# Performance work log

Hardware: AMD Instinct MI355X
Metric: run time of the kernel (lower is better)

Reference implementation:

```python
import jax, jax.numpy as jnp
import numpy as np

B, H, N, D = 4, 16, 2048, 64

def setup_inputs() -> dict:
    key = jax.random.key(0)
    kq, kk, kv = jax.random.split(key, 3)
    q = jax.random.normal(kq, (B, H, N, D), dtype=jnp.float32)
    k = jax.random.normal(kk, (B, H, N, D), dtype=jnp.float32)
    v = jax.random.normal(kv, (B, H, N, D), dtype=jnp.float32)
    return {"q": q, "k": k, "v": v}

def reference(q, k, v):
    scale = q.shape[-1] ** -0.5
    # sim: [b, h, i, j]
    sim = jnp.einsum('bhid,bhjd->bhij', q, k) * scale
    attn = jax.nn.softmax(sim, axis=-1)  # dropout p=0.0 -> identity
    out = jnp.einsum('bhij,bhjd->bhid', attn, v)
    return out
```

## Files before the change

### kernel.cpp

```cpp
#include <hip/hip_runtime.h>
#include <stdint.h>


#define NSEQ 2048
#define DH   64
#define BHN  64
#define NIT  32

typedef short bf16x8 __attribute__((ext_vector_type(8)));
typedef float f32x4  __attribute__((ext_vector_type(4)));
typedef float f32x16 __attribute__((ext_vector_type(16)));

__device__ __forceinline__ uint16_t f2bf(float x) {
    uint32_t u = __builtin_bit_cast(uint32_t, x);
    return (uint16_t)((u + 0x7fffu + ((u >> 16) & 1u)) >> 16);
}
__device__ __forceinline__ uint32_t pk2(float a, float b) {
    return (uint32_t)f2bf(a) | ((uint32_t)f2bf(b) << 16);
}

__global__ __launch_bounds__(256) void prepass(const float* __restrict__ K,
                                               const float* __restrict__ V,
                                               uint16_t* __restrict__ F) {
    __shared__ float T1[64 * 68];
    const int b = blockIdx.x, bh = b >> 5, kt = b & 31, t = threadIdx.x;
    const size_t gbase = ((size_t)bh * NSEQ + (size_t)kt * 64) * DH;
    const int n = t >> 2, d0 = (t & 3) * 16;
    #pragma unroll
    for (int i = 0; i < 4; ++i)
        *(float4*)&T1[n * 68 + d0 + i * 4] = *(const float4*)(V + gbase + n * 64 + d0 + i * 4);
    __syncthreads();
    uint16_t* out = F + (size_t)(bh * 32 + kt) * 8192;
    #pragma unroll
    for (int p = 0; p < 4; ++p) {
        const int e = p * 256 + t, c = e >> 6, l = e & 63;
        const int ll = l & 31, hh = l >> 5;
        float f[8];
        if (c < 8) {
            const int row = (c >> 2) * 32 + ll;
            const int col = hh * 8 + (c & 3) * 16;
            const float* kp = K + gbase + (size_t)row * 64 + col;
            float4 a = *(const float4*)(kp);
            float4 g = *(const float4*)(kp + 4);
            f[0] = a.x; f[1] = a.y; f[2] = a.z; f[3] = a.w;
            f[4] = g.x; f[5] = g.y; f[6] = g.z; f[7] = g.w;
        } else {
            const int cc = c - 8, ktg = cc >> 1;
            const int d = (cc & 1) * 32 + ll;
            #pragma unroll
            for (int j = 0; j < 8; ++j) {
                const int i = hh * 8 + j;
                const int s = (i & 3) + 8 * ((i >> 2) & 1) + 4 * ((i >> 3) & 1);
                f[j] = T1[(ktg * 16 + s) * 68 + d];
            }
        }
        uint4 o = make_uint4(pk2(f[0], f[1]), pk2(f[2], f[3]),
                             pk2(f[4], f[5]), pk2(f[6], f[7]));
        *(uint4*)(out + (size_t)c * 512 + l * 8) = o;
    }
}

__device__ __forceinline__ void load_q(const float* qp, float qscale, bf16x8 (&dst)[4]) {
    #pragma unroll
    for (int k2 = 0; k2 < 4; ++k2) {
        float4 a = *(const float4*)(qp + k2 * 16);
        float4 c = *(const float4*)(qp + k2 * 16 + 4);
        union { uint32_t u[4]; bf16x8 v; } pk;
        pk.u[0] = pk2(a.x * qscale, a.y * qscale);
        pk.u[1] = pk2(a.z * qscale, a.w * qscale);
        pk.u[2] = pk2(c.x * qscale, c.y * qscale);
        pk.u[3] = pk2(c.z * qscale, c.w * qscale);
        dst[k2] = pk.v;
    }
}

__device__ __forceinline__ void tile_nt(const uint4 (&kc)[4], const uint4 (&vc)[4],
                                        const bf16x8 (&qfn)[4],
                                        f32x16& o0, f32x16& o1, float& lsn) {
    f32x16 s = {};
    #pragma unroll
    for (int k2 = 0; k2 < 4; ++k2)
        s = __builtin_amdgcn_mfma_f32_32x32x16_bf16(
            __builtin_bit_cast(bf16x8, kc[k2]), qfn[k2], s, 0, 0, 0);
    bf16x8 pf0, pf1;
    float ls = 0.0f;
    {
        union { uint32_t u[4]; bf16x8 v; } pp;
        #pragma unroll
        for (int t2 = 0; t2 < 4; ++t2) {
            float e0 = __builtin_amdgcn_exp2f(s[2 * t2]);
            float e1 = __builtin_amdgcn_exp2f(s[2 * t2 + 1]);
            ls += e0 + e1;
            pp.u[t2] = __builtin_amdgcn_perm(
                __builtin_bit_cast(uint32_t, e1),
                __builtin_bit_cast(uint32_t, e0), 0x07060302u);
        }
        pf0 = pp.v;
    }
    {
        union { uint32_t u[4]; bf16x8 v; } pp;
        #pragma unroll
        for (int t2 = 0; t2 < 4; ++t2) {
            float e0 = __builtin_amdgcn_exp2f(s[8 + 2 * t2]);
            float e1 = __builtin_amdgcn_exp2f(s[8 + 2 * t2 + 1]);
            ls += e0 + e1;
            pp.u[t2] = __builtin_amdgcn_perm(
                __builtin_bit_cast(uint32_t, e1),
                __builtin_bit_cast(uint32_t, e0), 0x07060302u);
        }
        pf1 = pp.v;
    }
    lsn += ls;
    o0 = __builtin_amdgcn_mfma_f32_32x32x16_bf16(
        pf0, __builtin_bit_cast(bf16x8, vc[0]), o0, 0, 0, 0);
    o0 = __builtin_amdgcn_mfma_f32_32x32x16_bf16(
        pf1, __builtin_bit_cast(bf16x8, vc[2]), o0, 0, 0, 0);
    o1 = __builtin_amdgcn_mfma_f32_32x32x16_bf16(
        pf0, __builtin_bit_cast(bf16x8, vc[1]), o1, 0, 0, 0);
    o1 = __builtin_amdgcn_mfma_f32_32x32x16_bf16(
        pf1, __builtin_bit_cast(bf16x8, vc[3]), o1, 0, 0, 0);
}

__device__ __forceinline__ void ep_store(float (*XOd)[64], float* XLd,
                                         const f32x16& a0, const f32x16& a1,
                                         float ls, int lane) {
    #pragma unroll
    for (int e = 0; e < 16; ++e) XOd[e][lane] = a0[e];
    #pragma unroll
    for (int e = 0; e < 16; ++e) XOd[16 + e][lane] = a1[e];
    XLd[lane] = ls;
}
__device__ __forceinline__ void ep_add(const float (*XOs)[64],
                                       f32x16& a0, f32x16& a1, int lane) {
    #pragma unroll
    for (int e = 0; e < 16; ++e) a0[e] += XOs[e][lane];
    #pragma unroll
    for (int e = 0; e < 16; ++e) a1[e] += XOs[16 + e][lane];
}
__device__ __forceinline__ void ep_write(float* Ob, int row0,
                                         const f32x16& a0, const f32x16& a1,
                                         float lt, int l31, int h) {
    const float rinv = 1.0f / lt;
    const int rib = __builtin_bit_cast(int, rinv);
    #pragma unroll
    for (int rg = 0; rg < 16; ++rg) {
        const int il = (rg & 3) + 8 * (rg >> 2) + 4 * h;
        const float inv = __builtin_bit_cast(float,
            __builtin_amdgcn_ds_bpermute(il * 4, rib));
        const int row = row0 + il;
        Ob[(size_t)row * DH + l31]      = a0[rg] * inv;
        Ob[(size_t)row * DH + 32 + l31] = a1[rg] * inv;
    }
}

__global__ __launch_bounds__(128, 3) void attn_main(const float* __restrict__ Qg,
                                                    const uint16_t* __restrict__ F,
                                                    float* __restrict__ Og) {
    __shared__ float XO[2][32][64];
    __shared__ float XL[2][64];
    const int tid = threadIdx.x;
    const int w = tid >> 6, lane = tid & 63;
    const int l31 = lane & 31, h = lane >> 5;
    const int idx = blockIdx.x;
    const int bh = (idx & 7) * 8 + ((idx >> 3) & 7);
    const int qt = idx >> 6;

    const float qscale = 0.125f * 1.44269504f;
    bf16x8 qf0[4], qf1[4];
    {
        const float* qb = Qg + ((size_t)bh * NSEQ + (size_t)(qt * 64 + l31)) * DH + h * 8;
        load_q(qb, qscale, qf0);
        load_q(qb + 32 * DH, qscale, qf1);
    }

    f32x16 oa00 = {}, oa01 = {}, oa10 = {}, oa11 = {};
    float ls0 = 0.0f, ls1 = 0.0f;

    const uint16_t* fb = F + (size_t)bh * 32 * 8192 + (size_t)w * 2048 + (size_t)lane * 8;

    #pragma unroll 1
    for (int kt = 0; kt < NIT; ++kt) {
        uint4 kc[4], vc[4];
        #pragma unroll
        for (int c = 0; c < 4; ++c) kc[c] = *(const uint4*)(fb + (size_t)c * 512);
        #pragma unroll
        for (int c = 0; c < 4; ++c) vc[c] = *(const uint4*)(fb + (size_t)(8 + c) * 512);
        fb += 8192;
        tile_nt(kc, vc, qf0, oa00, oa01, ls0);
        tile_nt(kc, vc, qf1, oa10, oa11, ls1);
    }

    if (w == 0) ep_store(XO[0], XL[0], oa10, oa11, ls1, lane);
    else        ep_store(XO[1], XL[1], oa00, oa01, ls0, lane);
    __syncthreads();
    float lt;
    if (w == 0) { ep_add(XO[1], oa00, oa01, lane); lt = ls0 + XL[1][lane]; }
    else        { ep_add(XO[0], oa10, oa11, lane); lt = ls1 + XL[0][lane]; }
    lt += __shfl_xor(lt, 32);

    float* Ob = Og + (size_t)bh * NSEQ * DH;
    if (w == 0) ep_write(Ob, qt * 64,      oa00, oa01, lt, l31, h);
    else        ep_write(Ob, qt * 64 + 32, oa10, oa11, lt, l31, h);
}

#define LDS_S 72
#define NWAVE 4
#define BN    64
__global__ __launch_bounds__(256) void attn_fwd_fb(const float* __restrict__ Qg,
                                                   const float* __restrict__ Kg,
                                                   const float* __restrict__ Vg,
                                                   float* __restrict__ Og) {
    __shared__ short KsF[BN * LDS_S];
    __shared__ short VtsF[DH * LDS_S];
    __shared__ short PsF[NWAVE * 16 * LDS_S];
    const int tid = threadIdx.x;
    const int wave = tid >> 6, lane = tid & 63, quad = lane >> 4, l16 = lane & 15;
    const int bh = blockIdx.x >> 5, qtf = blockIdx.x & 31;
    const size_t base = (size_t)bh * NSEQ * DH;
    const float* Qb = Qg + base; const float* Kbf = Kg + base;
    const float* Vb = Vg + base; float* Ob = Og + base;
    const float qscale = 0.125f * 1.44269504f;
    bf16x8 qfrag[2];
    {
        const int qrow = qtf * 64 + wave * 16 + l16;
        const float* qp = Qb + (size_t)qrow * DH + quad * 8;
        #pragma unroll
        for (int c = 0; c < 2; ++c) {
            float4 x = *(const float4*)(qp + 32 * c);
            float4 y = *(const float4*)(qp + 32 * c + 4);
            union { uint16_t u[8]; bf16x8 v; } pk;
            pk.u[0]=f2bf(x.x*qscale); pk.u[1]=f2bf(x.y*qscale);
            pk.u[2]=f2bf(x.z*qscale); pk.u[3]=f2bf(x.w*qscale);
            pk.u[4]=f2bf(y.x*qscale); pk.u[5]=f2bf(y.y*qscale);
            pk.u[6]=f2bf(y.z*qscale); pk.u[7]=f2bf(y.w*qscale);
            qfrag[c] = pk.v;
        }
    }
    f32x4 o[4] = {};
    float m_i[4], l_i[4];
    #pragma unroll
    for (int r = 0; r < 4; ++r) { m_i[r] = -1e30f; l_i[r] = 0.0f; }
    const int kr0 = tid >> 4, kd0 = (tid & 15) * 4;
    const int vp = (tid & 31) * 2, vd0 = (tid >> 5) * 8;
    #pragma unroll 1
    for (int kt = 0; kt < NSEQ / BN; ++kt) {
        __syncthreads();
        {
            const float* kbase = Kbf + (size_t)kt * BN * DH;
            #pragma unroll
            for (int jj = 0; jj < 4; ++jj) {
                const int row = kr0 + jj * 16;
                float4 x = *(const float4*)(kbase + (size_t)row * DH + kd0);
                union { uint16_t u[4]; uint64_t ll; } pk;
                pk.u[0]=f2bf(x.x); pk.u[1]=f2bf(x.y); pk.u[2]=f2bf(x.z); pk.u[3]=f2bf(x.w);
                *(uint64_t*)&KsF[row * LDS_S + kd0] = pk.ll;
            }
        }
        {
            const float* v0 = Vb + (size_t)(kt * BN + vp) * DH + vd0;
            const float* v1 = v0 + DH;
            float4 a0 = *(const float4*)(v0); float4 a1 = *(const float4*)(v0 + 4);
            float4 b0 = *(const float4*)(v1); float4 b1 = *(const float4*)(v1 + 4);
            float av[8] = {a0.x,a0.y,a0.z,a0.w,a1.x,a1.y,a1.z,a1.w};
            float bv[8] = {b0.x,b0.y,b0.z,b0.w,b1.x,b1.y,b1.z,b1.w};
            #pragma unroll
            for (int i = 0; i < 8; ++i)
                *(uint32_t*)&VtsF[(vd0 + i) * LDS_S + vp] = pk2(av[i], bv[i]);
        }
        __syncthreads();
        f32x4 s[4] = {};
        #pragma unroll
        for (int c = 0; c < 2; ++c)
            #pragma unroll
            for (int n = 0; n < 4; ++n) {
                bf16x8 kfr = *(const bf16x8*)&KsF[(n * 16 + l16) * LDS_S + quad * 8 + 32 * c];
                s[n] = __builtin_amdgcn_mfma_f32_16x16x32_bf16(qfrag[c], kfr, s[n], 0, 0, 0);
            }
        float rmax[4];
        #pragma unroll
        for (int r = 0; r < 4; ++r)
            rmax[r] = fmaxf(fmaxf(s[0][r], s[1][r]), fmaxf(s[2][r], s[3][r]));
        #pragma unroll
        for (int off = 1; off < 16; off <<= 1)
            #pragma unroll
            for (int r = 0; r < 4; ++r)
                rmax[r] = fmaxf(rmax[r], __shfl_xor(rmax[r], off, 64));
        float alpha[4], rsum[4];
        #pragma unroll
        for (int r = 0; r < 4; ++r) {
            float mn = fmaxf(m_i[r], rmax[r]);
            alpha[r] = __builtin_amdgcn_exp2f(m_i[r] - mn);
            m_i[r] = mn; rsum[r] = 0.0f;
        }
        #pragma unroll
        for (int n = 0; n < 4; ++n)
            #pragma unroll
            for (int r = 0; r < 4; ++r) {
                float p = __builtin_amdgcn_exp2f(s[n][r] - m_i[r]);
                rsum[r] += p;
                PsF[(wave * 16 + quad * 4 + r) * LDS_S + n * 16 + l16] = (short)f2bf(p);
            }
        #pragma unroll
        for (int off = 1; off < 16; off <<= 1)
            #pragma unroll
            for (int r = 0; r < 4; ++r)
                rsum[r] += __shfl_xor(rsum[r], off, 64);
        #pragma unroll
        for (int r = 0; r < 4; ++r) l_i[r] = l_i[r] * alpha[r] + rsum[r];
        #pragma unroll
        for (int n = 0; n < 4; ++n)
            #pragma unroll
            for (int r = 0; r < 4; ++r) o[n][r] *= alpha[r];
        #pragma unroll
        for (int c = 0; c < 2; ++c) {
            bf16x8 pfr = *(const bf16x8*)&PsF[(wave * 16 + l16) * LDS_S + quad * 8 + 32 * c];
            #pragma unroll
            for (int n = 0; n < 4; ++n) {
                bf16x8 vfr = *(const bf16x8*)&VtsF[(n * 16 + l16) * LDS_S + quad * 8 + 32 * c];
                o[n] = __builtin_amdgcn_mfma_f32_16x16x32_bf16(pfr, vfr, o[n], 0, 0, 0);
            }
        }
    }
    float inv[4];
    #pragma unroll
    for (int r = 0; r < 4; ++r) inv[r] = 1.0f / l_i[r];
    const int orow0 = qtf * 64 + wave * 16 + quad * 4;
    #pragma unroll
    for (int n = 0; n < 4; ++n)
        #pragma unroll
        for (int r = 0; r < 4; ++r)
            Ob[(size_t)(orow0 + r) * DH + n * 16 + l16] = o[n][r] * inv[r];
}

extern "C" void kernel_launch(void* const* d_in, const int* in_sizes, int n_in,
                              void* d_out, int out_size, void* d_ws, size_t ws_size,
                              hipStream_t stream) {
    (void)in_sizes; (void)n_in; (void)out_size;
    const float* q = (const float*)d_in[0];
    const float* k = (const float*)d_in[1];
    const float* v = (const float*)d_in[2];
    float* out = (float*)d_out;
    const size_t need = (size_t)BHN * 32 * 16384;
    if (ws_size >= need) {
        uint16_t* fbuf = (uint16_t*)d_ws;
        prepass<<<dim3(BHN * 32), dim3(256), 0, stream>>>(k, v, fbuf);
        attn_main<<<dim3(2048), dim3(128), 0, stream>>>(q, fbuf, out);
    } else {
        attn_fwd_fb<<<dim3(BHN * 32), dim3(256), 0, stream>>>(q, k, v, out);
    }
}
```

Measured before the change: 210.0 us.

## Split query rows across waves instead of key tiles, dropping LDS reduction

Each wave now owns 32 query rows and walks all keys in the tile, rather than both waves sharing the query rows and splitting the key tile. This removes the shared-memory partial-sum exchange and the barrier in the epilogue, and halves the Q fragments and accumulators held per wave. In exchange each wave loads twice as much K/V per iteration, doubling global/L2 traffic per block and raising register pressure for the loaded tiles. The row-sum is also accumulated as a tree to shorten the dependency chain.

New measurement: 208.3 us. No clear change (-0.8%).

```diff
diff --git a/kernel.cpp b/kernel.cpp
--- a/kernel.cpp
+++ b/kernel.cpp
@@ -74,43 +74,45 @@
     }
 }
 
-__device__ __forceinline__ void tile_nt(const uint4 (&kc)[4], const uint4 (&vc)[4],
-                                        const bf16x8 (&qfn)[4],
-                                        f32x16& o0, f32x16& o1, float& lsn) {
+__device__ __forceinline__ void tile_mtj(const uint4 (&kc)[4], const uint4 (&vc)[4],
+                                         const bf16x8 (&qfn)[4],
+                                         f32x16& o0, f32x16& o1, float& lsn) {
     f32x16 s = {};
     #pragma unroll
     for (int k2 = 0; k2 < 4; ++k2)
         s = __builtin_amdgcn_mfma_f32_32x32x16_bf16(
             __builtin_bit_cast(bf16x8, kc[k2]), qfn[k2], s, 0, 0, 0);
     bf16x8 pf0, pf1;
-    float ls = 0.0f;
+    float g0, g1;
     {
         union { uint32_t u[4]; bf16x8 v; } pp;
+        float e[8];
         #pragma unroll
         for (int t2 = 0; t2 < 4; ++t2) {
-            float e0 = __builtin_amdgcn_exp2f(s[2 * t2]);
-            float e1 = __builtin_amdgcn_exp2f(s[2 * t2 + 1]);
-            ls += e0 + e1;
+            e[2 * t2]     = __builtin_amdgcn_exp2f(s[2 * t2]);
+            e[2 * t2 + 1] = __builtin_amdgcn_exp2f(s[2 * t2 + 1]);
             pp.u[t2] = __builtin_amdgcn_perm(
-                __builtin_bit_cast(uint32_t, e1),
-                __builtin_bit_cast(uint32_t, e0), 0x07060302u);
-        }
+                __builtin_bit_cast(uint32_t, e[2 * t2 + 1]),
+                __builtin_bit_cast(uint32_t, e[2 * t2]), 0x07060302u);
+        }
+        g0 = ((e[0] + e[1]) + (e[2] + e[3])) + ((e[4] + e[5]) + (e[6] + e[7]));
         pf0 = pp.v;
     }
     {
         union { uint32_t u[4]; bf16x8 v; } pp;
+        float e[8];
         #pragma unroll
         for (int t2 = 0; t2 < 4; ++t2) {
-            float e0 = __builtin_amdgcn_exp2f(s[8 + 2 * t2]);
-            float e1 = __builtin_amdgcn_exp2f(s[8 + 2 * t2 + 1]);
-            ls += e0 + e1;
+            e[2 * t2]     = __builtin_amdgcn_exp2f(s[8 + 2 * t2]);
+            e[2 * t2 + 1] = __builtin_amdgcn_exp2f(s[8 + 2 * t2 + 1]);
             pp.u[t2] = __builtin_amdgcn_perm(
-                __builtin_bit_cast(uint32_t, e1),
-                __builtin_bit_cast(uint32_t, e0), 0x07060302u);
-        }
+                __builtin_bit_cast(uint32_t, e[2 * t2 + 1]),
+                __builtin_bit_cast(uint32_t, e[2 * t2]), 0x07060302u);
+        }
+        g1 = ((e[0] + e[1]) + (e[2] + e[3])) + ((e[4] + e[5]) + (e[6] + e[7]));
         pf1 = pp.v;
     }
-    lsn += ls;
+    lsn += g0 + g1;
     o0 = __builtin_amdgcn_mfma_f32_32x32x16_bf16(
         pf0, __builtin_bit_cast(bf16x8, vc[0]), o0, 0, 0, 0);
     o0 = __builtin_amdgcn_mfma_f32_32x32x16_bf16(
@@ -121,22 +123,6 @@
         pf1, __builtin_bit_cast(bf16x8, vc[3]), o1, 0, 0, 0);
 }
 
-__device__ __forceinline__ void ep_store(float (*XOd)[64], float* XLd,
-                                         const f32x16& a0, const f32x16& a1,
-                                         float ls, int lane) {
-    #pragma unroll
-    for (int e = 0; e < 16; ++e) XOd[e][lane] = a0[e];
-    #pragma unroll
-    for (int e = 0; e < 16; ++e) XOd[16 + e][lane] = a1[e];
-    XLd[lane] = ls;
-}
-__device__ __forceinline__ void ep_add(const float (*XOs)[64],
-                                       f32x16& a0, f32x16& a1, int lane) {
-    #pragma unroll
-    for (int e = 0; e < 16; ++e) a0[e] += XOs[e][lane];
-    #pragma unroll
-    for (int e = 0; e < 16; ++e) a1[e] += XOs[16 + e][lane];
-}
 __device__ __forceinline__ void ep_write(float* Ob, int row0,
                                          const f32x16& a0, const f32x16& a1,
                                          float lt, int l31, int h) {
@@ -156,8 +142,6 @@
 __global__ __launch_bounds__(128, 3) void attn_main(const float* __restrict__ Qg,
                                                     const uint16_t* __restrict__ F,
                                                     float* __restrict__ Og) {
-    __shared__ float XO[2][32][64];
-    __shared__ float XL[2][64];
     const int tid = threadIdx.x;
     const int w = tid >> 6, lane = tid & 63;
     const int l31 = lane & 31, h = lane >> 5;
@@ -166,41 +150,34 @@
     const int qt = idx >> 6;
 
     const float qscale = 0.125f * 1.44269504f;
-    bf16x8 qf0[4], qf1[4];
-    {
-        const float* qb = Qg + ((size_t)bh * NSEQ + (size_t)(qt * 64 + l31)) * DH + h * 8;
-        load_q(qb, qscale, qf0);
-        load_q(qb + 32 * DH, qscale, qf1);
-    }
-
-    f32x16 oa00 = {}, oa01 = {}, oa10 = {}, oa11 = {};
-    float ls0 = 0.0f, ls1 = 0.0f;
-
-    const uint16_t* fb = F + (size_t)bh * 32 * 8192 + (size_t)w * 2048 + (size_t)lane * 8;
+    bf16x8 qf[4];
+    load_q(Qg + ((size_t)bh * NSEQ + (size_t)(qt * 64 + w * 32 + l31)) * DH + h * 8,
+           qscale, qf);
+
+    f32x16 oa0 = {}, oa1 = {};
+    float ls = 0.0f;
+
+    const uint16_t* fb = F + (size_t)bh * 32 * 8192 + (size_t)lane * 8;
 
     #pragma unroll 1
     for (int kt = 0; kt < NIT; ++kt) {
-        uint4 kc[4], vc[4];
-        #pragma unroll
-        for (int c = 0; c < 4; ++c) kc[c] = *(const uint4*)(fb + (size_t)c * 512);
-        #pragma unroll
-        for (int c = 0; c < 4; ++c) vc[c] = *(const uint4*)(fb + (size_t)(8 + c) * 512);
+        uint4 kcl[4], kch[4], vcl[4], vch[4];
+        #pragma unroll
+        for (int c = 0; c < 4; ++c) kcl[c] = *(const uint4*)(fb + (size_t)c * 512);
+        #pragma unroll
+        for (int c = 0; c < 4; ++c) kch[c] = *(const uint4*)(fb + (size_t)(4 + c) * 512);
+        #pragma unroll
+        for (int c = 0; c < 4; ++c) vcl[c] = *(const uint4*)(fb + (size_t)(8 + c) * 512);
+        #pragma unroll
+        for (int c = 0; c < 4; ++c) vch[c] = *(const uint4*)(fb + (size_t)(12 + c) * 512);
         fb += 8192;
-        tile_nt(kc, vc, qf0, oa00, oa01, ls0);
-        tile_nt(kc, vc, qf1, oa10, oa11, ls1);
-    }
-
-    if (w == 0) ep_store(XO[0], XL[0], oa10, oa11, ls1, lane);
-    else        ep_store(XO[1], XL[1], oa00, oa01, ls0, lane);
-    __syncthreads();
-    float lt;
-    if (w == 0) { ep_add(XO[1], oa00, oa01, lane); lt = ls0 + XL[1][lane]; }
-    else        { ep_add(XO[0], oa10, oa11, lane); lt = ls1 + XL[0][lane]; }
-    lt += __shfl_xor(lt, 32);
-
+        tile_mtj(kcl, vcl, qf, oa0, oa1, ls);
+        tile_mtj(kch, vch, qf, oa0, oa1, ls);
+    }
+
+    float lt = ls + __shfl_xor(ls, 32);
     float* Ob = Og + (size_t)bh * NSEQ * DH;
-    if (w == 0) ep_write(Ob, qt * 64,      oa00, oa01, lt, l31, h);
-    else        ep_write(Ob, qt * 64 + 32, oa10, oa11, lt, l31, h);
+    ep_write(Ob, qt * 64 + w * 32, oa0, oa1, lt, l31, h);
 }
 
 #define LDS_S 72
```
